# Kernel tuning notes

Hardware: AMD Instinct MI355X
Metric: run time of the kernel (lower is better)

Reference implementation:

```python
import jax, jax.numpy as jnp
import numpy as np

D_MODEL = 768
N_HEADS = 12
D_K = D_MODEL // N_HEADS
NEG_INF = -1e9


def setup_inputs() -> dict:
    key = jax.random.key(0)
    ks = jax.random.split(key, 7)
    B, S = 4, 2048
    x = jax.random.normal(ks[0], (B, S, D_MODEL), dtype=jnp.float32)
    # causal mask, broadcastable to [B, H, S, S]
    mask = jnp.tril(jnp.ones((S, S), dtype=bool))[None, None, :, :]
    scale = 1.0 / np.sqrt(D_MODEL)
    Wq = jax.random.normal(ks[1], (D_MODEL, D_MODEL), dtype=jnp.float32) * scale
    bq = jnp.zeros((D_MODEL,), dtype=jnp.float32)
    Wk = jax.random.normal(ks[2], (D_MODEL, D_MODEL), dtype=jnp.float32) * scale
    bk = jnp.zeros((D_MODEL,), dtype=jnp.float32)
    Wv = jax.random.normal(ks[3], (D_MODEL, D_MODEL), dtype=jnp.float32) * scale
    bv = jnp.zeros((D_MODEL,), dtype=jnp.float32)
    return {"x": x, "mask": mask, "Wq": Wq, "bq": bq, "Wk": Wk, "bk": bk, "Wv": Wv, "bv": bv}


def reference(x, mask, Wq, bq, Wk, bk, Wv, bv):
    B, S, _ = x.shape
    # projections (torch Linear: y = x @ W.T + b)
    q = (x @ Wq.T + bq).reshape(B, S, N_HEADS, D_K)
    k = (x @ Wk.T + bk).reshape(B, S, N_HEADS, D_K)
    v = (x @ Wv.T + bv).reshape(B, S, N_HEADS, D_K)
    # scores: [B, H, S, S]
    scores = jnp.einsum("bqhd,bkhd->bhqk", q, k) / jnp.sqrt(jnp.float32(D_K))
    scores = jnp.where(mask, scores, NEG_INF)
    probs = jax.nn.softmax(scores, axis=-1)
    # attention: [B, H, S, D_K] -> [B, S, d_model]
    attn = jnp.einsum("bhqk,bkhd->bqhd", probs, v).reshape(B, S, D_MODEL)
    return attn
```

## Files before the change

### kernel.cpp

```cpp
#include <hip/hip_runtime.h>
#include <math.h>


#define S_LEN 2048
#define BATCH 4
#define HEADS 12
#define DM 768
#define DK 64
#define BH (BATCH*HEADS)
#define MROWS (BATCH*S_LEN)
#define QSCALE 0.1803368801111244f

typedef __attribute__((ext_vector_type(8))) short short8;
typedef __attribute__((ext_vector_type(4))) float floatx4;
typedef __attribute__((address_space(3))) unsigned char lds_byte;
typedef __attribute__((address_space(1))) const unsigned char glob_byte;

__device__ __forceinline__ unsigned short f2bf(float f) {
  union { float f; unsigned int u; } a; a.f = f;
  unsigned int u = a.u;
  return (unsigned short)((u + 0x7fffu + ((u >> 16) & 1u)) >> 16);
}
__device__ __forceinline__ unsigned short f2bf_rtz(float f) {
  union { float f; unsigned int u; } a; a.f = f;
  return (unsigned short)(a.u >> 16);
}

__global__ void cast_all(const float* __restrict__ x,
                         const float* __restrict__ w0, const float* __restrict__ w1,
                         const float* __restrict__ w2,
                         unsigned short* __restrict__ xb,
                         unsigned short* __restrict__ wb) {
  const int NXB = (MROWS * DM) / 1024;
  const int NWB = (DM * DM) / 1024;
  int id = blockIdx.x;
  const float* src;
  unsigned short* dst;
  int blk;
  if (id < NXB) { src = x; dst = xb; blk = id; }
  else {
    int t = id - NXB, m = t / NWB;
    blk = t - m * NWB;
    src = (m == 0) ? w0 : (m == 1) ? w1 : w2;
    dst = wb + (size_t)m * (DM * DM);
  }
  int i = (blk * 256 + threadIdx.x) * 4;
  float4 v = *(const float4*)(src + i);
  ushort4 o;
  o.x = f2bf(v.x); o.y = f2bf(v.y); o.z = f2bf(v.z); o.w = f2bf(v.w);
  *(ushort4*)(dst + i) = o;
}

__global__ __launch_bounds__(256) void qkv_gemm(
    const unsigned short* __restrict__ xb,
    const unsigned short* __restrict__ wb,
    const float* __restrict__ bq, const float* __restrict__ bk,
    const float* __restrict__ bv,
    unsigned short* __restrict__ qo,
    unsigned short* __restrict__ ko,
    unsigned short* __restrict__ vto) {
  __shared__ unsigned short a_lds[2 * 128 * 32];
  __shared__ unsigned short b_lds[2 * 128 * 32];
  const int mat = blockIdx.z;
  const int tid = threadIdx.x;
  const int wave = tid >> 6, lane = tid & 63, quad = lane >> 4, ln = lane & 15;
  const int wm = wave & 1, wn = wave >> 1;
  const int m_blk = blockIdx.x * 128, n_blk = blockIdx.y * 128;
  const unsigned short* w = wb + (size_t)mat * DM * DM;
  const int srow_i[2] = { (0 * 256 + wave * 64 + lane) >> 2,
                          (1 * 256 + wave * 64 + lane) >> 2 };
  const int sq = (lane & 3) * 8;

  const floatx4 fz = {0.f, 0.f, 0.f, 0.f};
  floatx4 acc[4][4];
#pragma unroll
  for (int mg = 0; mg < 4; mg++)
#pragma unroll
    for (int c = 0; c < 4; c++) acc[mg][c] = fz;

  for (int k0 = 0; k0 < DM; k0 += 64) {
#pragma unroll
    for (int p = 0; p < 2; p++)
#pragma unroll
      for (int i = 0; i < 2; i++) {
        const int cbase = i * 256 + wave * 64;
        const int row = srow_i[i];
        __builtin_amdgcn_global_load_lds(
            (glob_byte*)(xb + (size_t)(m_blk + row) * DM + k0 + p * 32 + sq),
            (lds_byte*)(a_lds + p * 4096 + cbase * 8), 16, 0, 0);
        __builtin_amdgcn_global_load_lds(
            (glob_byte*)(w + (size_t)(n_blk + row) * DM + k0 + p * 32 + sq),
            (lds_byte*)(b_lds + p * 4096 + cbase * 8), 16, 0, 0);
      }
    __syncthreads();

    short8 af[4][2], bf[4][2];
#pragma unroll
    for (int mg = 0; mg < 4; mg++)
#pragma unroll
      for (int p = 0; p < 2; p++)
        af[mg][p] = *(const short8*)(a_lds + p * 4096 + (wm * 64 + mg * 16 + ln) * 32 + quad * 8);
#pragma unroll
    for (int c = 0; c < 4; c++)
#pragma unroll
      for (int p = 0; p < 2; p++)
        bf[c][p] = *(const short8*)(b_lds + p * 4096 + (wn * 64 + c * 16 + ln) * 32 + quad * 8);
#pragma unroll
    for (int mg = 0; mg < 4; mg++)
#pragma unroll
      for (int c = 0; c < 4; c++) {
        acc[mg][c] = __builtin_amdgcn_mfma_f32_16x16x32_bf16(af[mg][0], bf[c][0], acc[mg][c], 0, 0, 0);
        acc[mg][c] = __builtin_amdgcn_mfma_f32_16x16x32_bf16(af[mg][1], bf[c][1], acc[mg][c], 0, 0, 0);
      }
    __syncthreads();
  }

  const float* bias = (mat == 0) ? bq : (mat == 1) ? bk : bv;
  const float oscale = (mat == 0) ? QSCALE : 1.0f;
  const int m_base = m_blk + wm * 64, n_base = n_blk + wn * 64;
#pragma unroll
  for (int mg = 0; mg < 4; mg++)
#pragma unroll
    for (int c = 0; c < 4; c++) {
      int gn = n_base + c * 16 + ln;
      int hd = gn >> 6, d = gn & 63;
      float bias_v = bias[gn] * oscale;
      int gm0 = m_base + mg * 16 + quad * 4;
      int bb = gm0 >> 11, s0 = gm0 & (S_LEN - 1);
      if (mat == 2) {
        ushort4 pk;
        pk.x = f2bf(acc[mg][c][0] + bias_v);
        pk.y = f2bf(acc[mg][c][1] + bias_v);
        pk.z = f2bf(acc[mg][c][2] + bias_v);
        pk.w = f2bf(acc[mg][c][3] + bias_v);
        *(ushort4*)(vto + (((size_t)(bb * HEADS + hd)) * DK + d) * S_LEN + s0) = pk;
      } else {
        unsigned short* dst = (mat == 0 ? qo : ko) +
            (((size_t)(bb * HEADS + hd)) * S_LEN + s0) * DK + d;
#pragma unroll
        for (int r = 0; r < 4; r++)
          dst[(size_t)r * DK] = f2bf(acc[mg][c][r] * oscale + bias_v);
      }
    }
}

__global__ __launch_bounds__(128) void flash_attn(
    const unsigned short* __restrict__ q,
    const unsigned short* __restrict__ k,
    const unsigned short* __restrict__ vt,
    float* __restrict__ out) {
  __shared__ unsigned short p_lds[2][32 * 128];
  const int id = blockIdx.x;
  const int bh = id % BH;
  const int qt = (S_LEN / 64 - 1) - (id / BH);
  const int q0 = qt * 64;
  const int tid = threadIdx.x;
  const int wave = tid >> 6, lane = tid & 63, quad = lane >> 4, ln = lane & 15;
  unsigned short* pl = p_lds[wave];
  const unsigned short* qp = q  + (size_t)bh * S_LEN * DK;
  const unsigned short* kp = k  + (size_t)bh * S_LEN * DK;
  const unsigned short* vp = vt + (size_t)bh * DK * S_LEN;
  const int qr_base = q0 + wave * 32;
  const floatx4 fz = {0.f, 0.f, 0.f, 0.f};

  unsigned short* wp[8];
#pragma unroll
  for (int kg = 0; kg < 8; kg++)
    wp[kg] = pl + quad * 512 + ((kg ^ quad) * 16) + ((ln >> 3) * 8) + (ln & 7);
  const unsigned short* rp[4];
#pragma unroll
  for (int ss = 0; ss < 4; ss++)
    rp[ss] = pl + ln * 128 + (((ss * 4 + quad) ^ (((ln >> 2) & 3) << 1)) * 8);

  const int klane = ln * DK + quad * 8;
  const int vlane = ln * S_LEN + quad * 8;

  short8 ones;
#pragma unroll
  for (int j = 0; j < 8; j++) ones[j] = (short)0x3F80;

  short8 aq[2][2];
#pragma unroll
  for (int h = 0; h < 2; h++)
#pragma unroll
    for (int ss = 0; ss < 2; ss++)
      aq[h][ss] = *(const short8*)(qp + (qr_base + h * 16 + ln) * DK + ss * 32 + quad * 8);

  floatx4 o[2][4];
  floatx4 ol[2] = {fz, fz};
#pragma unroll
  for (int h = 0; h < 2; h++) {
    o[h][0] = fz; o[h][1] = fz; o[h][2] = fz; o[h][3] = fz;
  }

  auto qk_phase = [&](int kbase, int kgbase) {
    short8 kf[4][2];
#pragma unroll
    for (int kg = 0; kg < 4; kg++)
#pragma unroll
      for (int ss = 0; ss < 2; ss++)
        kf[kg][ss] = *(const short8*)(kp + klane + (kbase + kg * 16) * DK + ss * 32);
    const bool domask = (kbase + 63 > qr_base);
#pragma unroll
    for (int h = 0; h < 2; h++) {
      floatx4 sc[4];
#pragma unroll
      for (int kg = 0; kg < 4; kg++) {
        floatx4 tt = __builtin_amdgcn_mfma_f32_16x16x32_bf16(aq[h][0], kf[kg][0], fz, 0, 0, 0);
        sc[kg] = __builtin_amdgcn_mfma_f32_16x16x32_bf16(aq[h][1], kf[kg][1], tt, 0, 0, 0);
      }
#pragma unroll
      for (int kg = 0; kg < 4; kg++) {
        int key = kbase + kg * 16 + ln;
#pragma unroll
        for (int r = 0; r < 4; r++) {
          float pv = exp2f(sc[kg][r]);
          if (domask) {
            int qr = qr_base + h * 16 + quad * 4 + r;
            pv = (key <= qr) ? pv : 0.f;
          }
          wp[kgbase + kg][h * 2048 + r * 128] = f2bf_rtz(pv);
        }
      }
    }
  };

  auto pv_phase = [&](int kbase, int nss) {
    for (int ss = 0; ss < nss; ss++) {
      short8 vf[4];
#pragma unroll
      for (int dg = 0; dg < 4; dg++)
        vf[dg] = *(const short8*)(vp + vlane + dg * 16 * S_LEN + kbase + ss * 32);
#pragma unroll
      for (int h = 0; h < 2; h++) {
        short8 ap = *(const short8*)(rp[ss] + h * 2048);
#pragma unroll
        for (int dg = 0; dg < 4; dg++)
          o[h][dg] = __builtin_amdgcn_mfma_f32_16x16x32_bf16(ap, vf[dg], o[h][dg], 0, 0, 0);
        ol[h] = __builtin_amdgcn_mfma_f32_16x16x32_bf16(ap, ones, ol[h], 0, 0, 0);
      }
    }
  };

  const int kend = qr_base + 32;
  int k0 = 0;
  for (; k0 + 128 <= kend; k0 += 128) {
    qk_phase(k0, 0);
    qk_phase(k0 + 64, 4);
    pv_phase(k0, 4);
  }
  for (; k0 < kend; k0 += 64) {
    qk_phase(k0, 0);
    pv_phase(k0, 2);
  }

  const int b = bh / HEADS, hd = bh % HEADS;
#pragma unroll
  for (int h = 0; h < 2; h++)
#pragma unroll
    for (int r = 0; r < 4; r++) {
      float inv = 1.f / ol[h][r];
      int qr = qr_base + h * 16 + quad * 4 + r;
      float* orow = out + ((size_t)(b * S_LEN + qr)) * DM + hd * DK;
      orow[ln]      = o[h][0][r] * inv;
      orow[16 + ln] = o[h][1][r] * inv;
      orow[32 + ln] = o[h][2][r] * inv;
      orow[48 + ln] = o[h][3][r] * inv;
    }
}

extern "C" void kernel_launch(void* const* d_in, const int* in_sizes, int n_in,
                              void* d_out, int out_size, void* d_ws, size_t ws_size,
                              hipStream_t stream) {
  const float* x  = (const float*)d_in[0];
  const float* Wq = (const float*)d_in[2];
  const float* bq = (const float*)d_in[3];
  const float* Wk = (const float*)d_in[4];
  const float* bk = (const float*)d_in[5];
  const float* Wv = (const float*)d_in[6];
  const float* bv = (const float*)d_in[7];
  float* out = (float*)d_out;

  const int NX = MROWS * DM;
  const int NW = DM * DM;
  unsigned short* xb = (unsigned short*)d_ws;
  unsigned short* wb = xb + NX;
  unsigned short* qo = wb + 3 * NW;
  unsigned short* ko = qo + (size_t)BH * S_LEN * DK;
  unsigned short* vt = ko + (size_t)BH * S_LEN * DK;

  cast_all<<<dim3(NX / 1024 + 3 * (NW / 1024)), 256, 0, stream>>>(
      x, Wq, Wk, Wv, xb, wb);

  qkv_gemm<<<dim3(MROWS / 128, DM / 128, 3), 256, 0, stream>>>(
      xb, wb, bq, bk, bv, qo, ko, vt);

  flash_attn<<<dim3((S_LEN / 64) * BH), 128, 0, stream>>>(qo, ko, vt, out);
}
```

Baseline: 255.8 us.

## Keep softmax probabilities in registers by transposing QK^T and using 16x16x16 MFMA

The scores are now computed as K·Q^T so each lane's MFMA output already matches the B-operand layout of a 16x16x16 bf16 MFMA. The P@V product then consumes the probabilities straight from registers, which removes the LDS round trip for P and its swizzled address setup. The cost is that P@V now uses the smaller-K MFMA, so it issues twice as many MFMA instructions. V is loaded as 4-element vectors each iteration instead of 8, and the output is stored as float4 per row.

```diff
diff --git a/kernel.cpp b/kernel.cpp
--- a/kernel.cpp
+++ b/kernel.cpp
@@ -12,6 +12,7 @@
 #define QSCALE 0.1803368801111244f
 
 typedef __attribute__((ext_vector_type(8))) short short8;
+typedef __attribute__((ext_vector_type(4))) short short4v;
 typedef __attribute__((ext_vector_type(4))) float floatx4;
 typedef __attribute__((address_space(3))) unsigned char lds_byte;
 typedef __attribute__((address_space(1))) const unsigned char glob_byte;
@@ -25,6 +26,23 @@
   union { float f; unsigned int u; } a; a.f = f;
   return (unsigned short)(a.u >> 16);
 }
+
+#if __has_builtin(__builtin_amdgcn_mfma_f32_16x16x16_bf16)
+__device__ __forceinline__ floatx4 mfma16(short4v a, short4v b, floatx4 c) {
+  return __builtin_amdgcn_mfma_f32_16x16x16_bf16(a, b, c, 0, 0, 0);
+}
+#elif __has_builtin(__builtin_amdgcn_mfma_f32_16x16x16bf16_1k)
+__device__ __forceinline__ floatx4 mfma16(short4v a, short4v b, floatx4 c) {
+  return __builtin_amdgcn_mfma_f32_16x16x16bf16_1k(a, b, c, 0, 0, 0);
+}
+#else
+__device__ __forceinline__ floatx4 mfma16(short4v a, short4v b, floatx4 c) {
+  floatx4 d;
+  asm("v_mfma_f32_16x16x16_bf16 %0, %1, %2, %3"
+      : "=v"(d) : "v"(a), "v"(b), "v"(c));
+  return d;
+}
+#endif
 
 __global__ void cast_all(const float* __restrict__ x,
                          const float* __restrict__ w0, const float* __restrict__ w1,
@@ -149,35 +167,24 @@
     const unsigned short* __restrict__ k,
     const unsigned short* __restrict__ vt,
     float* __restrict__ out) {
-  __shared__ unsigned short p_lds[2][32 * 128];
   const int id = blockIdx.x;
   const int bh = id % BH;
   const int qt = (S_LEN / 64 - 1) - (id / BH);
   const int q0 = qt * 64;
   const int tid = threadIdx.x;
   const int wave = tid >> 6, lane = tid & 63, quad = lane >> 4, ln = lane & 15;
-  unsigned short* pl = p_lds[wave];
   const unsigned short* qp = q  + (size_t)bh * S_LEN * DK;
   const unsigned short* kp = k  + (size_t)bh * S_LEN * DK;
   const unsigned short* vp = vt + (size_t)bh * DK * S_LEN;
   const int qr_base = q0 + wave * 32;
   const floatx4 fz = {0.f, 0.f, 0.f, 0.f};
 
-  unsigned short* wp[8];
-#pragma unroll
-  for (int kg = 0; kg < 8; kg++)
-    wp[kg] = pl + quad * 512 + ((kg ^ quad) * 16) + ((ln >> 3) * 8) + (ln & 7);
-  const unsigned short* rp[4];
-#pragma unroll
-  for (int ss = 0; ss < 4; ss++)
-    rp[ss] = pl + ln * 128 + (((ss * 4 + quad) ^ (((ln >> 2) & 3) << 1)) * 8);
-
   const int klane = ln * DK + quad * 8;
-  const int vlane = ln * S_LEN + quad * 8;
-
-  short8 ones;
-#pragma unroll
-  for (int j = 0; j < 8; j++) ones[j] = (short)0x3F80;
+  const int vlane = ln * S_LEN + quad * 4;
+
+  short4v ones4;
+#pragma unroll
+  for (int j = 0; j < 4; j++) ones4[j] = (short)0x3F80;
 
   short8 aq[2][2];
 #pragma unroll
@@ -193,80 +200,60 @@
     o[h][0] = fz; o[h][1] = fz; o[h][2] = fz; o[h][3] = fz;
   }
 
-  auto qk_phase = [&](int kbase, int kgbase) {
+  const int kend = qr_base + 32;
+  for (int kbase = 0; kbase < kend; kbase += 64) {
     short8 kf[4][2];
 #pragma unroll
-    for (int kg = 0; kg < 4; kg++)
+    for (int kk = 0; kk < 4; kk++)
 #pragma unroll
       for (int ss = 0; ss < 2; ss++)
-        kf[kg][ss] = *(const short8*)(kp + klane + (kbase + kg * 16) * DK + ss * 32);
+        kf[kk][ss] = *(const short8*)(kp + klane + (kbase + kk * 16) * DK + ss * 32);
+
     const bool domask = (kbase + 63 > qr_base);
 #pragma unroll
-    for (int h = 0; h < 2; h++) {
-      floatx4 sc[4];
-#pragma unroll
-      for (int kg = 0; kg < 4; kg++) {
-        floatx4 tt = __builtin_amdgcn_mfma_f32_16x16x32_bf16(aq[h][0], kf[kg][0], fz, 0, 0, 0);
-        sc[kg] = __builtin_amdgcn_mfma_f32_16x16x32_bf16(aq[h][1], kf[kg][1], tt, 0, 0, 0);
-      }
-#pragma unroll
-      for (int kg = 0; kg < 4; kg++) {
-        int key = kbase + kg * 16 + ln;
+    for (int kk = 0; kk < 4; kk++) {
+      short4v vf[4];
+#pragma unroll
+      for (int dg = 0; dg < 4; dg++)
+        vf[dg] = *(const short4v*)(vp + vlane + dg * 16 * S_LEN + kbase + kk * 16);
+
+#pragma unroll
+      for (int h = 0; h < 2; h++) {
+        floatx4 sc = __builtin_amdgcn_mfma_f32_16x16x32_bf16(kf[kk][0], aq[h][0], fz, 0, 0, 0);
+        sc = __builtin_amdgcn_mfma_f32_16x16x32_bf16(kf[kk][1], aq[h][1], sc, 0, 0, 0);
+
+        short4v bq;
 #pragma unroll
         for (int r = 0; r < 4; r++) {
-          float pv = exp2f(sc[kg][r]);
+          float pv = exp2f(sc[r]);
           if (domask) {
-            int qr = qr_base + h * 16 + quad * 4 + r;
+            int key = kbase + kk * 16 + quad * 4 + r;
+            int qr = qr_base + h * 16 + ln;
             pv = (key <= qr) ? pv : 0.f;
           }
-          wp[kgbase + kg][h * 2048 + r * 128] = f2bf_rtz(pv);
+          bq[r] = (short)f2bf_rtz(pv);
         }
+#pragma unroll
+        for (int dg = 0; dg < 4; dg++)
+          o[h][dg] = mfma16(vf[dg], bq, o[h][dg]);
+        ol[h] = mfma16(ones4, bq, ol[h]);
       }
     }
-  };
-
-  auto pv_phase = [&](int kbase, int nss) {
-    for (int ss = 0; ss < nss; ss++) {
-      short8 vf[4];
-#pragma unroll
-      for (int dg = 0; dg < 4; dg++)
-        vf[dg] = *(const short8*)(vp + vlane + dg * 16 * S_LEN + kbase + ss * 32);
-#pragma unroll
-      for (int h = 0; h < 2; h++) {
-        short8 ap = *(const short8*)(rp[ss] + h * 2048);
-#pragma unroll
-        for (int dg = 0; dg < 4; dg++)
-          o[h][dg] = __builtin_amdgcn_mfma_f32_16x16x32_bf16(ap, vf[dg], o[h][dg], 0, 0, 0);
-        ol[h] = __builtin_amdgcn_mfma_f32_16x16x32_bf16(ap, ones, ol[h], 0, 0, 0);
-      }
+  }
+
+  const int b = bh / HEADS, hd = bh % HEADS;
+#pragma unroll
+  for (int h = 0; h < 2; h++) {
+    float inv = 1.f / ol[h][0];
+    float* orow = out + ((size_t)(b * S_LEN + qr_base + h * 16 + ln)) * DM + hd * DK;
+#pragma unroll
+    for (int dg = 0; dg < 4; dg++) {
+      float4 v4;
+      v4.x = o[h][dg][0] * inv; v4.y = o[h][dg][1] * inv;
+      v4.z = o[h][dg][2] * inv; v4.w = o[h][dg][3] * inv;
+      *(float4*)(orow + dg * 16 + quad * 4) = v4;
     }
-  };
-
-  const int kend = qr_base + 32;
-  int k0 = 0;
-  for (; k0 + 128 <= kend; k0 += 128) {
-    qk_phase(k0, 0);
-    qk_phase(k0 + 64, 4);
-    pv_phase(k0, 4);
-  }
-  for (; k0 < kend; k0 += 64) {
-    qk_phase(k0, 0);
-    pv_phase(k0, 2);
-  }
-
-  const int b = bh / HEADS, hd = bh % HEADS;
-#pragma unroll
-  for (int h = 0; h < 2; h++)
-#pragma unroll
-    for (int r = 0; r < 4; r++) {
-      float inv = 1.f / ol[h][r];
-      int qr = qr_base + h * 16 + quad * 4 + r;
-      float* orow = out + ((size_t)(b * S_LEN + qr)) * DM + hd * DK;
-      orow[ln]      = o[h][0][r] * inv;
-      orow[16 + ln] = o[h][1][r] * inv;
-      orow[32 + ln] = o[h][2][r] * inv;
-      orow[48 + ln] = o[h][3][r] * inv;
-    }
+  }
 }
 
 extern "C" void kernel_launch(void* const* d_in, const int* in_sizes, int n_in,
```

After: 310.6 us. +21.4%, slower.
